# Performance work log

Measured on AMD Instinct MI355X. Metric: run time of the kernel, lower is better.

The kernel has to match this reference:

```python
import jax, jax.numpy as jnp
import numpy as np

NEG_SLOPE = 0.2  # PyG GATConv default negative_slope


def _glorot(key, shape):
    fan = shape[0]
    return jax.random.normal(key, shape, dtype=jnp.float32) / np.sqrt(fan)


def setup_inputs() -> dict:
    key = jax.random.key(0)
    ks = jax.random.split(key, 32)
    N, E, C_IN, C_H, C_OUT = 20000, 320000, 128, 640, 2
    inp = {
        "x": jax.random.normal(ks[0], (N, C_IN), dtype=jnp.float32),
        "edge_index": jax.random.randint(ks[1], (2, E), 0, N, dtype=jnp.int64),
    }
    dims = [(C_IN, C_H), (C_H, C_H), (C_H, C_H), (C_H, C_H), (C_H, C_OUT)]
    for i, (ci, co) in enumerate(dims, start=1):
        k = jax.random.split(ks[1 + i], 4)
        inp[f"W{i}"] = _glorot(k[0], (ci, co))
        inp[f"as{i}"] = _glorot(k[1], (co,))
        inp[f"ad{i}"] = _glorot(k[2], (co,))
        inp[f"b{i}"] = jnp.zeros((co,), dtype=jnp.float32)
    return inp


def _gat_conv(h, W, a_src, a_dst, b, src, dst, N):
    # h: [N, Ci] -> hW: [N, Co]
    hW = h @ W
    # per-edge attention logit: LeakyReLU(alpha_src[j] + alpha_dst[i]) for edge j->i
    e = jax.nn.leaky_relu((hW @ a_src)[src] + (hW @ a_dst)[dst], NEG_SLOPE)
    # segment softmax over incoming edges of each dst node (self-loops guarantee nonempty)
    m = jax.ops.segment_max(e, dst, num_segments=N)
    ex = jnp.exp(e - m[dst])
    den = jax.ops.segment_sum(ex, dst, num_segments=N)
    alpha = ex / den[dst]
    # weighted scatter-add of source messages
    out = jax.ops.segment_sum(alpha[:, None] * hW[src], dst, num_segments=N)
    return out + b


def reference(x, edge_index, W1, as1, ad1, b1, W2, as2, ad2, b2, W3, as3, ad3, b3,
              W4, as4, ad4, b4, W5, as5, ad5, b5):
    N = x.shape[0]
    # PyG GATConv default add_self_loops=True
    loops = jnp.arange(N, dtype=edge_index.dtype)
    ei = jnp.concatenate([edge_index, jnp.stack([loops, loops])], axis=1)
    src, dst = ei[0], ei[1]
    h = jax.nn.relu(_gat_conv(x, W1, as1, ad1, b1, src, dst, N))
    h = jax.nn.relu(_gat_conv(h, W2, as2, ad2, b2, src, dst, N))
    h = jax.nn.relu(_gat_conv(h, W3, as3, ad3, b3, src, dst, N))
    h = jax.nn.relu(_gat_conv(h, W4, as4, ad4, b4, src, dst, N))
    # dropout in eval mode = identity
    return _gat_conv(h, W5, as5, ad5, b5, src, dst, N)
```

## Files before the change

kernel.cpp:

```cpp
#include <hip/hip_runtime.h>
#include <math.h>

#define N_NODES 20000
#define MPAD 20096
#define E_EDGES 320000
#define ET (E_EDGES + N_NODES)
#define C_HID 640
#define NEG_SLOPE 0.2f

typedef __attribute__((ext_vector_type(8))) short bf16x8;
typedef __attribute__((ext_vector_type(4))) float f32x4;

__device__ __forceinline__ float leaky(float x) { return x > 0.f ? x : NEG_SLOPE * x; }

__device__ __forceinline__ unsigned short f2bf(float f) {
    unsigned u = __float_as_uint(f);
    unsigned r = (u + 0x7fffu + ((u >> 16) & 1u)) >> 16;
    return (unsigned short)r;
}
__device__ __forceinline__ float bf2f(unsigned short h) {
    return __uint_as_float(((unsigned)h) << 16);
}

__device__ __forceinline__ void gld16(const void* g, void* l) {
    __builtin_amdgcn_global_load_lds((const __attribute__((address_space(1))) unsigned int*)g,
                                     (__attribute__((address_space(3))) unsigned int*)l,
                                     16, 0, 0);
}

__global__ void k_zero(int* p, int n) {
    int i = blockIdx.x * blockDim.x + threadIdx.x;
    if (i < n) p[i] = 0;
}

__global__ void k_zerof(float* p, int n) {
    int i = blockIdx.x * blockDim.x + threadIdx.x;
    if (i < n) p[i] = 0.f;
}

__global__ void k_count(const int* __restrict__ ei, int* __restrict__ counts) {
    int j = blockIdx.x * blockDim.x + threadIdx.x;
    if (j >= ET) return;
    int d = (j < E_EDGES) ? ei[E_EDGES + j] : (j - E_EDGES);
    atomicAdd(&counts[d], 1);
}

__global__ __launch_bounds__(1024) void k_scan(const int* __restrict__ counts,
                                               int* __restrict__ rowptr) {
    __shared__ int part[1024];
    int t = threadIdx.x;
    int base = t * 20;
    int incl[20];
    int s = 0;
#pragma unroll
    for (int k = 0; k < 20; k++) {
        int i = base + k;
        int v = (i < N_NODES) ? counts[i] : 0;
        s += v;
        incl[k] = s;
    }
    part[t] = s;
    __syncthreads();
    for (int off = 1; off < 1024; off <<= 1) {
        int x = (t >= off) ? part[t - off] : 0;
        __syncthreads();
        part[t] += x;
        __syncthreads();
    }
    int prefix = (t == 0) ? 0 : part[t - 1];
    if (t == 0) rowptr[0] = 0;
#pragma unroll
    for (int k = 0; k < 20; k++) {
        int i = base + k;
        if (i < N_NODES) rowptr[i + 1] = prefix + incl[k];
    }
}

__global__ void k_copy(const int* __restrict__ a, int* __restrict__ b, int n) {
    int i = blockIdx.x * blockDim.x + threadIdx.x;
    if (i < n) b[i] = a[i];
}

__global__ void k_fill(const int* __restrict__ ei, int* __restrict__ cursor, int* __restrict__ col) {
    int j = blockIdx.x * blockDim.x + threadIdx.x;
    if (j >= ET) return;
    int s, d;
    if (j < E_EDGES) { s = ei[j]; d = ei[E_EDGES + j]; }
    else { s = d = j - E_EDGES; }
    int pos = atomicAdd(&cursor[d], 1);
    col[pos] = s;
}

__global__ void k_splitx(const float* __restrict__ x, unsigned short* __restrict__ xh,
                         unsigned short* __restrict__ xl) {
    int idx = blockIdx.x * blockDim.x + threadIdx.x;
    if (idx >= MPAD * 128 / 4) return;
    int row = idx >> 5;
    float4 v = make_float4(0.f, 0.f, 0.f, 0.f);
    if (row < N_NODES) v = ((const float4*)x)[idx];
    float a[4] = {v.x, v.y, v.z, v.w};
    unsigned short h[4], l[4];
#pragma unroll
    for (int i = 0; i < 4; i++) {
        h[i] = f2bf(a[i]);
        l[i] = f2bf(a[i] - bf2f(h[i]));
    }
    *(ushort4*)&xh[idx * 4] = make_ushort4(h[0], h[1], h[2], h[3]);
    *(ushort4*)&xl[idx * 4] = make_ushort4(l[0], l[1], l[2], l[3]);
}

__global__ void k_splitW(const float* __restrict__ W, unsigned short* __restrict__ Wth,
                         unsigned short* __restrict__ Wtl, int K) {
    int idx = blockIdx.x * blockDim.x + threadIdx.x;
    if (idx >= K * C_HID) return;
    int k = idx / C_HID, n = idx - k * C_HID;
    float w = W[idx];
    unsigned short h = f2bf(w);
    Wth[n * K + k] = h;
    Wtl[n * K + k] = f2bf(w - bf2f(h));
}

__global__ void k_padzero(unsigned short* __restrict__ ph, unsigned short* __restrict__ pl) {
    int idx = blockIdx.x * blockDim.x + threadIdx.x;
    int total = (MPAD - N_NODES) * C_HID;
    if (idx >= total) return;
    ph[N_NODES * C_HID + idx] = 0;
    pl[N_NODES * C_HID + idx] = 0;
}

__global__ __launch_bounds__(256) void k_mfma_gemm(
    const unsigned short* __restrict__ Ahi, const unsigned short* __restrict__ Alo,
    const unsigned short* __restrict__ Bth, const unsigned short* __restrict__ Btl,
    float* __restrict__ C, int K, int M,
    const float* __restrict__ asrc, const float* __restrict__ adst,
    float* __restrict__ as_, float* __restrict__ ad_) {
    __shared__ unsigned short lds[4 * 128 * 32];
    const int t = threadIdx.x;
    const int lane = t & 63, wv = t >> 6;
    const int wm = wv & 1, wn = wv >> 1;
    const int quad = lane >> 4, cl = lane & 15;
    const int rowBase = blockIdx.x * 128;
    const int colBase = blockIdx.y * 128;
    const int r = t >> 2, c8 = (t & 3) * 8;

    f32x4 acc[4][4];
#pragma unroll
    for (int i = 0; i < 4; i++)
#pragma unroll
        for (int j = 0; j < 4; j++)
            acc[i][j] = (f32x4){0.f, 0.f, 0.f, 0.f};

    for (int k0 = 0; k0 < K; k0 += 32) {
        __syncthreads();
#pragma unroll
        for (int p = 0; p < 2; ++p) {
            int row = p * 64 + r;
            size_t ga = (size_t)(rowBase + row) * K + k0 + c8;
            size_t gb = (size_t)(colBase + row) * K + k0 + c8;
            int lo = row * 32 + c8;
            gld16(Ahi + ga, &lds[lo]);
            gld16(Alo + ga, &lds[4096 + lo]);
            gld16(Bth + gb, &lds[8192 + lo]);
            gld16(Btl + gb, &lds[12288 + lo]);
        }
        __syncthreads();

        bf16x8 ah[4], al[4], bh[4], bl[4];
#pragma unroll
        for (int i = 0; i < 4; ++i) {
            int am = (wm * 64 + i * 16 + cl) * 32 + quad * 8;
            ah[i] = *(const bf16x8*)&lds[am];
            al[i] = *(const bf16x8*)&lds[4096 + am];
            int bn = (wn * 64 + i * 16 + cl) * 32 + quad * 8;
            bh[i] = *(const bf16x8*)&lds[8192 + bn];
            bl[i] = *(const bf16x8*)&lds[12288 + bn];
        }
#pragma unroll
        for (int i = 0; i < 4; ++i)
#pragma unroll
            for (int j = 0; j < 4; ++j) {
                acc[i][j] = __builtin_amdgcn_mfma_f32_16x16x32_bf16(ah[i], bh[j], acc[i][j], 0, 0, 0);
                acc[i][j] = __builtin_amdgcn_mfma_f32_16x16x32_bf16(ah[i], bl[j], acc[i][j], 0, 0, 0);
                acc[i][j] = __builtin_amdgcn_mfma_f32_16x16x32_bf16(al[i], bh[j], acc[i][j], 0, 0, 0);
            }
    }

#pragma unroll
    for (int i = 0; i < 4; ++i)
#pragma unroll
        for (int j = 0; j < 4; ++j) {
            int colC = colBase + wn * 64 + j * 16 + cl;
#pragma unroll
            for (int rr = 0; rr < 4; ++rr) {
                int rowC = rowBase + wm * 64 + i * 16 + quad * 4 + rr;
                if (rowC < M) C[(size_t)rowC * C_HID + colC] = acc[i][j][rr];
            }
        }

    float av[4], dv[4];
#pragma unroll
    for (int j = 0; j < 4; ++j) {
        int cn = colBase + wn * 64 + j * 16 + cl;
        av[j] = asrc[cn];
        dv[j] = adst[cn];
    }
#pragma unroll
    for (int i = 0; i < 4; ++i)
#pragma unroll
        for (int rr = 0; rr < 4; ++rr) {
            float s = 0.f, d = 0.f;
#pragma unroll
            for (int j = 0; j < 4; ++j) {
                float v = acc[i][j][rr];
                s = fmaf(v, av[j], s);
                d = fmaf(v, dv[j], d);
            }
#pragma unroll
            for (int o = 8; o >= 1; o >>= 1) {
                s += __shfl_xor(s, o);
                d += __shfl_xor(d, o);
            }
            int rowC = rowBase + wm * 64 + i * 16 + quad * 4 + rr;
            if (cl == 0 && rowC < M) {
                atomicAdd(&as_[rowC], s);
                atomicAdd(&ad_[rowC], d);
            }
        }
}

__global__ __launch_bounds__(256) void k_gather(const float* __restrict__ hW,
                                                const float* __restrict__ as_,
                                                const float* __restrict__ ad_,
                                                const int* __restrict__ rowptr,
                                                const int* __restrict__ col,
                                                const float* __restrict__ bias,
                                                unsigned short* __restrict__ outh,
                                                unsigned short* __restrict__ outl) {
    int wv = threadIdx.x >> 6, lane = threadIdx.x & 63;
    int node = blockIdx.x * 4 + wv;
    int c = blockIdx.y;
    if (node >= N_NODES) return;
    int start = rowptr[node], end = rowptr[node + 1];
    int deg = end - start;
    const float* base = hW + c * 128 + lane * 2;
    float ax = 0.f, ay = 0.f;
    float adi = ad_[node];

    if (deg <= 64) {
        int col_v = col[start + min(lane, deg - 1)];
        float asv = as_[col_v];
        float logit = (lane < deg) ? leaky(asv + adi) : -1e30f;
        float m = logit;
#pragma unroll
        for (int o = 32; o; o >>= 1) m = fmaxf(m, __shfl_xor(m, o));
        float ex = __expf(logit - m);
        float den = ex;
#pragma unroll
        for (int o = 32; o; o >>= 1) den += __shfl_xor(den, o);
        float alpha_v = ex / den;

        for (int e0 = 0; e0 < deg; e0 += 8) {
            float2 r[8];
            float a[8];
#pragma unroll
            for (int q = 0; q < 8; ++q) {
                int e = e0 + q;
                int ec = min(e, deg - 1);
                int s = __shfl(col_v, ec);
                float ar = __shfl(alpha_v, ec);
                a[q] = (e < deg) ? ar : 0.f;
                r[q] = *(const float2*)(base + (size_t)s * C_HID);
            }
#pragma unroll
            for (int q = 0; q < 8; ++q) {
                ax = fmaf(a[q], r[q].x, ax);
                ay = fmaf(a[q], r[q].y, ay);
            }
        }
    } else {
        float m = -1e30f;
        for (int j = start + lane; j < end; j += 64)
            m = fmaxf(m, leaky(as_[col[j]] + adi));
        for (int o = 32; o; o >>= 1) m = fmaxf(m, __shfl_xor(m, o));
        float den = 0.f;
        for (int j = start + lane; j < end; j += 64)
            den += __expf(leaky(as_[col[j]] + adi) - m);
        for (int o = 32; o; o >>= 1) den += __shfl_xor(den, o);
        float inv = 1.f / den;
        for (int j = start; j < end; ++j) {
            int s = col[j];
            float a = __expf(leaky(as_[s] + adi) - m) * inv;
            float2 r = *(const float2*)(base + (size_t)s * C_HID);
            ax = fmaf(a, r.x, ax);
            ay = fmaf(a, r.y, ay);
        }
    }

    float2 b = *(const float2*)&bias[c * 128 + lane * 2];
    float v0 = fmaxf(ax + b.x, 0.f);
    float v1 = fmaxf(ay + b.y, 0.f);
    unsigned short h0 = f2bf(v0), h1 = f2bf(v1);
    size_t o = (size_t)node * C_HID + c * 128 + lane * 2;
    *(ushort2*)&outh[o] = make_ushort2(h0, h1);
    *(ushort2*)&outl[o] = make_ushort2(f2bf(v0 - bf2f(h0)), f2bf(v1 - bf2f(h1)));
}

__global__ __launch_bounds__(256) void k_gemm2(const unsigned short* __restrict__ hh,
                                               const unsigned short* __restrict__ hl,
                                               const float* __restrict__ W,
                                               float* __restrict__ hW5) {
    int wave = (blockIdx.x * blockDim.x + threadIdx.x) >> 6;
    int lane = threadIdx.x & 63;
    if (wave >= N_NODES) return;
    const unsigned short* rh = hh + (size_t)wave * C_HID;
    const unsigned short* rl = hl + (size_t)wave * C_HID;
    float a0 = 0.f, a1 = 0.f;
#pragma unroll
    for (int k = lane; k < C_HID; k += 64) {
        float v = bf2f(rh[k]) + bf2f(rl[k]);
        a0 = fmaf(v, W[k * 2 + 0], a0);
        a1 = fmaf(v, W[k * 2 + 1], a1);
    }
    for (int o = 32; o; o >>= 1) { a0 += __shfl_xor(a0, o); a1 += __shfl_xor(a1, o); }
    if (lane == 0) { hW5[wave * 2 + 0] = a0; hW5[wave * 2 + 1] = a1; }
}

__global__ void k_logits2(const float* __restrict__ hW5, const float* __restrict__ asrc,
                          const float* __restrict__ adst,
                          float* __restrict__ as_, float* __restrict__ ad_) {
    int n = blockIdx.x * blockDim.x + threadIdx.x;
    if (n >= N_NODES) return;
    float h0 = hW5[n * 2], h1 = hW5[n * 2 + 1];
    as_[n] = h0 * asrc[0] + h1 * asrc[1];
    ad_[n] = h0 * adst[0] + h1 * adst[1];
}

__global__ void k_agg2(const float* __restrict__ hW5, const float* __restrict__ as_,
                       const float* __restrict__ ad_, const int* __restrict__ rowptr,
                       const int* __restrict__ col, const float* __restrict__ bias,
                       float* __restrict__ out) {
    int i = blockIdx.x * blockDim.x + threadIdx.x;
    if (i >= N_NODES) return;
    int start = rowptr[i], end = rowptr[i + 1];
    float adi = ad_[i];
    float m = -1e30f;
    for (int j = start; j < end; j++) m = fmaxf(m, leaky(as_[col[j]] + adi));
    float den = 0.f;
    for (int j = start; j < end; j++) den += __expf(leaky(as_[col[j]] + adi) - m);
    float inv = 1.f / den;
    float o0 = 0.f, o1 = 0.f;
    for (int j = start; j < end; j++) {
        int s = col[j];
        float al = __expf(leaky(as_[s] + adi) - m) * inv;
        o0 = fmaf(al, hW5[s * 2 + 0], o0);
        o1 = fmaf(al, hW5[s * 2 + 1], o1);
    }
    out[i * 2 + 0] = o0 + bias[0];
    out[i * 2 + 1] = o1 + bias[1];
}

extern "C" void kernel_launch(void* const* d_in, const int* in_sizes, int n_in,
                              void* d_out, int out_size, void* d_ws, size_t ws_size,
                              hipStream_t stream) {
    const float* x   = (const float*)d_in[0];
    const int*   ei  = (const int*)d_in[1];
    const float* W[5]  = {(const float*)d_in[2],  (const float*)d_in[6],
                          (const float*)d_in[10], (const float*)d_in[14],
                          (const float*)d_in[18]};
    const float* As[5] = {(const float*)d_in[3],  (const float*)d_in[7],
                          (const float*)d_in[11], (const float*)d_in[15],
                          (const float*)d_in[19]};
    const float* Ad[5] = {(const float*)d_in[4],  (const float*)d_in[8],
                          (const float*)d_in[12], (const float*)d_in[16],
                          (const float*)d_in[20]};
    const float* Bi[5] = {(const float*)d_in[5],  (const float*)d_in[9],
                          (const float*)d_in[13], (const float*)d_in[17],
                          (const float*)d_in[21]};
    float* out = (float*)d_out;

    char* w = (char*)d_ws;
    float* bufX = (float*)w;                 w += (size_t)N_NODES * C_HID * 4;
    unsigned short* pair_hi = (unsigned short*)w; w += (size_t)MPAD * C_HID * 2;
    unsigned short* pair_lo = (unsigned short*)w; w += (size_t)MPAD * C_HID * 2;
    unsigned short* Wth = (unsigned short*)w;     w += (size_t)C_HID * C_HID * 2;
    unsigned short* Wtl = (unsigned short*)w;     w += (size_t)C_HID * C_HID * 2;
    float* as_  = (float*)w;  w += N_NODES * 4;
    float* ad_  = (float*)w;  w += N_NODES * 4;
    float* hW5  = (float*)w;  w += N_NODES * 2 * 4;
    int* rowptr = (int*)w;    w += (N_NODES + 1) * 4 + 12;
    int* counts = (int*)w;    w += N_NODES * 4;
    int* col    = (int*)w;    w += ET * 4;

    const int TB = 256;
    k_zero<<<(N_NODES + TB - 1) / TB, TB, 0, stream>>>(counts, N_NODES);
    k_count<<<(ET + TB - 1) / TB, TB, 0, stream>>>(ei, counts);
    k_scan<<<1, 1024, 0, stream>>>(counts, rowptr);
    k_copy<<<(N_NODES + TB - 1) / TB, TB, 0, stream>>>(rowptr, counts, N_NODES);
    k_fill<<<(ET + TB - 1) / TB, TB, 0, stream>>>(ei, counts, col);

    k_padzero<<<((MPAD - N_NODES) * C_HID + TB - 1) / TB, TB, 0, stream>>>(pair_hi, pair_lo);
    k_splitx<<<(MPAD * 128 / 4 + TB - 1) / TB, TB, 0, stream>>>(x, pair_hi, pair_lo);

    dim3 gemmGrid(MPAD / 128, C_HID / 128);
    dim3 gathGrid(N_NODES / 4, 5);
    int nodeWaveBlocks = (N_NODES + 3) / 4;

    for (int l = 0; l <= 3; ++l) {
        int K = (l == 0) ? 128 : C_HID;
        k_zerof<<<(2 * N_NODES + TB - 1) / TB, TB, 0, stream>>>(as_, 2 * N_NODES);
        k_splitW<<<(K * C_HID + TB - 1) / TB, TB, 0, stream>>>(W[l], Wth, Wtl, K);
        k_mfma_gemm<<<gemmGrid, TB, 0, stream>>>(pair_hi, pair_lo, Wth, Wtl, bufX, K, N_NODES,
                                                 As[l], Ad[l], as_, ad_);
        k_gather<<<gathGrid, TB, 0, stream>>>(bufX, as_, ad_, rowptr, col, Bi[l], pair_hi, pair_lo);
    }

    k_gemm2<<<nodeWaveBlocks, TB, 0, stream>>>(pair_hi, pair_lo, W[4], hW5);
    k_logits2<<<(N_NODES + TB - 1) / TB, TB, 0, stream>>>(hW5, As[4], Ad[4], as_, ad_);
    k_agg2<<<(N_NODES + TB - 1) / TB, TB, 0, stream>>>(hW5, as_, ad_, rowptr, col, Bi[4], out);
}
```

Before: 881.1 us.

## Widen gather column chunks, double-buffer edge loads, make final aggregation wave-per-node

The per-layer gather now covers 640 columns with 3 blockIdx.y slices (256, 256, 128 columns) instead of 5 slices of 128. The wider slices use float4 loads, so the softmax over each node's edges is recomputed fewer times. Edge-row loads are double-buffered in groups of 8 to overlap memory latency with the FMAs, and launch bounds now request 4 blocks per SM. The final 2-channel aggregation changes from one thread per node to one wave per node with lane-parallel edges and shuffle reductions, which removes serial per-thread loops and their load divergence. The added register pressure may lower occupancy.

```diff
diff --git a/kernel.cpp b/kernel.cpp
--- a/kernel.cpp
+++ b/kernel.cpp
@@ -228,23 +228,25 @@
         }
 }
 
-__global__ __launch_bounds__(256) void k_gather(const float* __restrict__ hW,
-                                                const float* __restrict__ as_,
-                                                const float* __restrict__ ad_,
-                                                const int* __restrict__ rowptr,
-                                                const int* __restrict__ col,
-                                                const float* __restrict__ bias,
-                                                unsigned short* __restrict__ outh,
-                                                unsigned short* __restrict__ outl) {
+__global__ __launch_bounds__(256, 4) void k_gather(const float* __restrict__ hW,
+                                                   const float* __restrict__ as_,
+                                                   const float* __restrict__ ad_,
+                                                   const int* __restrict__ rowptr,
+                                                   const int* __restrict__ col,
+                                                   const float* __restrict__ bias,
+                                                   unsigned short* __restrict__ outh,
+                                                   unsigned short* __restrict__ outl) {
     int wv = threadIdx.x >> 6, lane = threadIdx.x & 63;
     int node = blockIdx.x * 4 + wv;
     int c = blockIdx.y;
     if (node >= N_NODES) return;
     int start = rowptr[node], end = rowptr[node + 1];
     int deg = end - start;
-    const float* base = hW + c * 128 + lane * 2;
-    float ax = 0.f, ay = 0.f;
     float adi = ad_[node];
+
+    float vout[4] = {0.f, 0.f, 0.f, 0.f};
+    int ncols = (c < 2) ? 4 : 2;
+    int cbase = c * 256;
 
     if (deg <= 64) {
         int col_v = col[start + min(lane, deg - 1)];
@@ -259,23 +261,78 @@
         for (int o = 32; o; o >>= 1) den += __shfl_xor(den, o);
         float alpha_v = ex / den;
 
-        for (int e0 = 0; e0 < deg; e0 += 8) {
-            float2 r[8];
-            float a[8];
-#pragma unroll
-            for (int q = 0; q < 8; ++q) {
-                int e = e0 + q;
-                int ec = min(e, deg - 1);
-                int s = __shfl(col_v, ec);
-                float ar = __shfl(alpha_v, ec);
-                a[q] = (e < deg) ? ar : 0.f;
-                r[q] = *(const float2*)(base + (size_t)s * C_HID);
-            }
-#pragma unroll
-            for (int q = 0; q < 8; ++q) {
-                ax = fmaf(a[q], r[q].x, ax);
-                ay = fmaf(a[q], r[q].y, ay);
-            }
+        if (c < 2) {
+            const float* base = hW + cbase + lane * 4;
+            float4 ra[8], rb[8];
+            float aa[8], ab[8];
+#define LOADG4(E0, R, A)                                                     \
+            {                                                                \
+                _Pragma("unroll")                                            \
+                for (int q = 0; q < 8; ++q) {                                \
+                    int e = (E0) + q;                                        \
+                    int ec = min(e, deg - 1);                                \
+                    int s = __shfl(col_v, ec);                               \
+                    float ar = __shfl(alpha_v, ec);                          \
+                    A[q] = (e < deg) ? ar : 0.f;                             \
+                    R[q] = *(const float4*)(base + (size_t)s * C_HID);       \
+                }                                                            \
+            }
+#define FMAG4(R, A)                                                          \
+            {                                                                \
+                _Pragma("unroll")                                            \
+                for (int q = 0; q < 8; ++q) {                                \
+                    vout[0] = fmaf(A[q], R[q].x, vout[0]);                   \
+                    vout[1] = fmaf(A[q], R[q].y, vout[1]);                   \
+                    vout[2] = fmaf(A[q], R[q].z, vout[2]);                   \
+                    vout[3] = fmaf(A[q], R[q].w, vout[3]);                   \
+                }                                                            \
+            }
+            int ng = (deg + 7) >> 3;
+            LOADG4(0, ra, aa);
+            int g = 1;
+            while (true) {
+                if (g >= ng) { FMAG4(ra, aa); break; }
+                LOADG4(g * 8, rb, ab); FMAG4(ra, aa); ++g;
+                if (g >= ng) { FMAG4(rb, ab); break; }
+                LOADG4(g * 8, ra, aa); FMAG4(rb, ab); ++g;
+            }
+#undef LOADG4
+#undef FMAG4
+        } else {
+            const float* base = hW + cbase + lane * 2;
+            float2 ra[8], rb[8];
+            float aa[8], ab[8];
+#define LOADG2(E0, R, A)                                                     \
+            {                                                                \
+                _Pragma("unroll")                                            \
+                for (int q = 0; q < 8; ++q) {                                \
+                    int e = (E0) + q;                                        \
+                    int ec = min(e, deg - 1);                                \
+                    int s = __shfl(col_v, ec);                               \
+                    float ar = __shfl(alpha_v, ec);                          \
+                    A[q] = (e < deg) ? ar : 0.f;                             \
+                    R[q] = *(const float2*)(base + (size_t)s * C_HID);       \
+                }                                                            \
+            }
+#define FMAG2(R, A)                                                          \
+            {                                                                \
+                _Pragma("unroll")                                            \
+                for (int q = 0; q < 8; ++q) {                                \
+                    vout[0] = fmaf(A[q], R[q].x, vout[0]);                   \
+                    vout[1] = fmaf(A[q], R[q].y, vout[1]);                   \
+                }                                                            \
+            }
+            int ng = (deg + 7) >> 3;
+            LOADG2(0, ra, aa);
+            int g = 1;
+            while (true) {
+                if (g >= ng) { FMAG2(ra, aa); break; }
+                LOADG2(g * 8, rb, ab); FMAG2(ra, aa); ++g;
+                if (g >= ng) { FMAG2(rb, ab); break; }
+                LOADG2(g * 8, ra, aa); FMAG2(rb, ab); ++g;
+            }
+#undef LOADG2
+#undef FMAG2
         }
     } else {
         float m = -1e30f;
@@ -287,22 +344,38 @@
             den += __expf(leaky(as_[col[j]] + adi) - m);
         for (int o = 32; o; o >>= 1) den += __shfl_xor(den, o);
         float inv = 1.f / den;
+        const float* base = hW + cbase + lane * ncols;
         for (int j = start; j < end; ++j) {
             int s = col[j];
             float a = __expf(leaky(as_[s] + adi) - m) * inv;
-            float2 r = *(const float2*)(base + (size_t)s * C_HID);
-            ax = fmaf(a, r.x, ax);
-            ay = fmaf(a, r.y, ay);
-        }
-    }
-
-    float2 b = *(const float2*)&bias[c * 128 + lane * 2];
-    float v0 = fmaxf(ax + b.x, 0.f);
-    float v1 = fmaxf(ay + b.y, 0.f);
-    unsigned short h0 = f2bf(v0), h1 = f2bf(v1);
-    size_t o = (size_t)node * C_HID + c * 128 + lane * 2;
-    *(ushort2*)&outh[o] = make_ushort2(h0, h1);
-    *(ushort2*)&outl[o] = make_ushort2(f2bf(v0 - bf2f(h0)), f2bf(v1 - bf2f(h1)));
+            if (c < 2) {
+                float4 r = *(const float4*)(base + (size_t)s * C_HID);
+                vout[0] = fmaf(a, r.x, vout[0]); vout[1] = fmaf(a, r.y, vout[1]);
+                vout[2] = fmaf(a, r.z, vout[2]); vout[3] = fmaf(a, r.w, vout[3]);
+            } else {
+                float2 r = *(const float2*)(base + (size_t)s * C_HID);
+                vout[0] = fmaf(a, r.x, vout[0]); vout[1] = fmaf(a, r.y, vout[1]);
+            }
+        }
+    }
+
+    size_t o = (size_t)node * C_HID + cbase + lane * ncols;
+    const float* bb = &bias[cbase + lane * ncols];
+    unsigned short hh[4], ll[4];
+#pragma unroll
+    for (int q = 0; q < 4; ++q) {
+        if (q >= ncols) break;
+        float v = fmaxf(vout[q] + bb[q], 0.f);
+        hh[q] = f2bf(v);
+        ll[q] = f2bf(v - bf2f(hh[q]));
+    }
+    if (c < 2) {
+        *(ushort4*)&outh[o] = make_ushort4(hh[0], hh[1], hh[2], hh[3]);
+        *(ushort4*)&outl[o] = make_ushort4(ll[0], ll[1], ll[2], ll[3]);
+    } else {
+        *(ushort2*)&outh[o] = make_ushort2(hh[0], hh[1]);
+        *(ushort2*)&outl[o] = make_ushort2(ll[0], ll[1]);
+    }
 }
 
 __global__ __launch_bounds__(256) void k_gemm2(const unsigned short* __restrict__ hh,
@@ -335,28 +408,59 @@
     ad_[n] = h0 * adst[0] + h1 * adst[1];
 }
 
-__global__ void k_agg2(const float* __restrict__ hW5, const float* __restrict__ as_,
-                       const float* __restrict__ ad_, const int* __restrict__ rowptr,
-                       const int* __restrict__ col, const float* __restrict__ bias,
-                       float* __restrict__ out) {
-    int i = blockIdx.x * blockDim.x + threadIdx.x;
-    if (i >= N_NODES) return;
-    int start = rowptr[i], end = rowptr[i + 1];
-    float adi = ad_[i];
-    float m = -1e30f;
-    for (int j = start; j < end; j++) m = fmaxf(m, leaky(as_[col[j]] + adi));
-    float den = 0.f;
-    for (int j = start; j < end; j++) den += __expf(leaky(as_[col[j]] + adi) - m);
-    float inv = 1.f / den;
-    float o0 = 0.f, o1 = 0.f;
-    for (int j = start; j < end; j++) {
-        int s = col[j];
-        float al = __expf(leaky(as_[s] + adi) - m) * inv;
-        o0 = fmaf(al, hW5[s * 2 + 0], o0);
-        o1 = fmaf(al, hW5[s * 2 + 1], o1);
-    }
-    out[i * 2 + 0] = o0 + bias[0];
-    out[i * 2 + 1] = o1 + bias[1];
+__global__ __launch_bounds__(256) void k_agg2(const float* __restrict__ hW5,
+                                              const float* __restrict__ as_,
+                                              const float* __restrict__ ad_,
+                                              const int* __restrict__ rowptr,
+                                              const int* __restrict__ col,
+                                              const float* __restrict__ bias,
+                                              float* __restrict__ out) {
+    int wv = threadIdx.x >> 6, lane = threadIdx.x & 63;
+    int node = blockIdx.x * 4 + wv;
+    if (node >= N_NODES) return;
+    int start = rowptr[node], end = rowptr[node + 1];
+    int deg = end - start;
+    float adi = ad_[node];
+    float o0, o1;
+    if (deg <= 64) {
+        int cv = col[start + min(lane, deg - 1)];
+        float logit = (lane < deg) ? leaky(as_[cv] + adi) : -1e30f;
+        float m = logit;
+#pragma unroll
+        for (int o = 32; o; o >>= 1) m = fmaxf(m, __shfl_xor(m, o));
+        float ex = __expf(logit - m);
+        float den = ex;
+#pragma unroll
+        for (int o = 32; o; o >>= 1) den += __shfl_xor(den, o);
+        float al = ex / den;
+        float2 hv = make_float2(0.f, 0.f);
+        if (lane < deg) hv = *(const float2*)&hW5[cv * 2];
+        o0 = al * hv.x; o1 = al * hv.y;
+#pragma unroll
+        for (int o = 32; o; o >>= 1) { o0 += __shfl_xor(o0, o); o1 += __shfl_xor(o1, o); }
+    } else {
+        float m = -1e30f;
+        for (int j = start + lane; j < end; j += 64)
+            m = fmaxf(m, leaky(as_[col[j]] + adi));
+        for (int o = 32; o; o >>= 1) m = fmaxf(m, __shfl_xor(m, o));
+        float den = 0.f;
+        for (int j = start + lane; j < end; j += 64)
+            den += __expf(leaky(as_[col[j]] + adi) - m);
+        for (int o = 32; o; o >>= 1) den += __shfl_xor(den, o);
+        float inv = 1.f / den;
+        o0 = 0.f; o1 = 0.f;
+        for (int j = start + lane; j < end; j += 64) {
+            int s = col[j];
+            float al = __expf(leaky(as_[s] + adi) - m) * inv;
+            o0 = fmaf(al, hW5[s * 2 + 0], o0);
+            o1 = fmaf(al, hW5[s * 2 + 1], o1);
+        }
+        for (int o = 32; o; o >>= 1) { o0 += __shfl_xor(o0, o); o1 += __shfl_xor(o1, o); }
+    }
+    if (lane == 0) {
+        out[node * 2 + 0] = o0 + bias[0];
+        out[node * 2 + 1] = o1 + bias[1];
+    }
 }
 
 extern "C" void kernel_launch(void* const* d_in, const int* in_sizes, int n_in,
@@ -402,7 +506,7 @@
     k_splitx<<<(MPAD * 128 / 4 + TB - 1) / TB, TB, 0, stream>>>(x, pair_hi, pair_lo);
 
     dim3 gemmGrid(MPAD / 128, C_HID / 128);
-    dim3 gathGrid(N_NODES / 4, 5);
+    dim3 gathGrid(N_NODES / 4, 3);
     int nodeWaveBlocks = (N_NODES + 3) / 4;
 
     for (int l = 0; l <= 3; ++l) {
@@ -416,5 +520,5 @@
 
     k_gemm2<<<nodeWaveBlocks, TB, 0, stream>>>(pair_hi, pair_lo, W[4], hW5);
     k_logits2<<<(N_NODES + TB - 1) / TB, TB, 0, stream>>>(hW5, As[4], Ad[4], as_, ad_);
-    k_agg2<<<(N_NODES + TB - 1) / TB, TB, 0, stream>>>(hW5, as_, ad_, rowptr, col, Bi[4], out);
-}
+    k_agg2<<<nodeWaveBlocks, TB, 0, stream>>>(hW5, as_, ad_, rowptr, col, Bi[4], out);
+}
```

Result: slower. 912.6 us (+3.6%).
